# Kernel optimization log

Hardware: AMD Instinct MI355X
Metric: run time of the kernel (lower is better)

## Reference

```python
import jax, jax.numpy as jnp
import numpy as np

N_NODES = 100000
N_EDGES = 3200000
IN_FEATS = 128
OUT_FEATS = 16
NEG_SLOPE = 0.2


def setup_inputs() -> dict:
    key = jax.random.key(0)
    k1, k2, k3, k4, k5, k6 = jax.random.split(key, 6)
    h = jax.random.normal(k1, (N_NODES, IN_FEATS), dtype=jnp.float32)
    src = jax.random.randint(k2, (N_EDGES,), 0, N_NODES, dtype=jnp.int64)
    dst = jax.random.randint(k3, (N_EDGES,), 0, N_NODES, dtype=jnp.int64)
    W = jax.random.normal(k4, (OUT_FEATS, IN_FEATS), dtype=jnp.float32) * (1.0 / np.sqrt(IN_FEATS))
    a_l = jax.random.normal(k5, (1, OUT_FEATS), dtype=jnp.float32) * (1.0 / np.sqrt(OUT_FEATS))
    a_r = jax.random.normal(k6, (1, OUT_FEATS), dtype=jnp.float32) * (1.0 / np.sqrt(OUT_FEATS))
    return {"h": h, "src": src, "dst": dst, "W": W, "a_l": a_l, "a_r": a_r}


def reference(h, src, dst, W, a_l, a_r):
    N = h.shape[0]
    # node projection: h @ fc.weight.T  -> [N, out]
    hW = h @ W.T
    # per-node attention logits: [N, 1]
    el = hW @ a_l.T
    er = hW @ a_r.T
    # u_add_v: per-edge logit e = el[src] + er[dst], then leaky_relu(0.2)
    e = jax.nn.leaky_relu(el[src] + er[dst], negative_slope=NEG_SLOPE)  # [E, 1]
    # edge_softmax over edges grouped by destination node (numerically stable)
    emax = jax.ops.segment_max(e, dst, num_segments=N)  # [N, 1], -inf for empty
    emax = jnp.where(jnp.isfinite(emax), emax, 0.0)
    e_exp = jnp.exp(e - emax[dst])
    esum = jax.ops.segment_sum(e_exp, dst, num_segments=N)  # [N, 1]
    alpha = e_exp / jnp.maximum(esum[dst], 1e-16)  # [E, 1]
    # u_mul_e + sum: weighted aggregation of source features at destinations
    out = jax.ops.segment_sum(hW[src] * alpha, dst, num_segments=N)  # [N, out]
    return out
```

## Files before the change

kernel.cpp:

```cpp
#include <hip/hip_runtime.h>
#include <hip/hip_bf16.h>
#include <stdint.h>

#define IN_F 128
#define OUT_F 16
#define NEG_SLOPE 0.2f
#define SB_BITS 9
#define SB_NODES 512
#define NBS 196
#define CAP_SB 17408
#define TILE_NODES 128
#define LCAP 4608
#define SC_E 4096
#define W_LD (IN_F + 4)
#define SB_SPACING 200

#define SMEM_BYTES (3136 + 16384 + 4096)

__global__ __launch_bounds__(256) void proj_scatter_kernel(
    const float* __restrict__ h, const float* __restrict__ W,
    const float* __restrict__ a_l, const float* __restrict__ a_r,
    const int* __restrict__ src, const int* __restrict__ dst,
    float* __restrict__ hW, float* __restrict__ el, float* __restrict__ er,
    int* __restrict__ cursor, uint32_t* __restrict__ payload,
    int N, int E, int scatBlocks) {
  __shared__ __align__(16) uint8_t smem[SMEM_BYTES];
  int t = threadIdx.x;

  if ((int)blockIdx.x < scatBlocks) {
    int* hist = (int*)smem;
    int* pref = hist + NBS;
    int* gbase = pref + NBS;
    int* rank = gbase + NBS;
    uint32_t* sortedP = (uint32_t*)(smem + 3136);
    uint8_t* sortedB = smem + 3136 + 16384;

    int start = blockIdx.x * SC_E;
    int end = min(E, start + SC_E);
    int cnt = end - start;

    if (t < NBS) { hist[t] = 0; rank[t] = 0; }
    __syncthreads();

    for (int i = start + t; i < end; i += 256)
      atomicAdd(&hist[dst[i] >> SB_BITS], 1);
    __syncthreads();

    if (t == 0) {
      int run = 0;
      for (int b = 0; b < NBS; ++b) {
        pref[b] = run;
        run += hist[b];
      }
    }
    __syncthreads();
    if (t < NBS) {
      int c = hist[t];
      gbase[t] = c ? atomicAdd(&cursor[t * 16], c) : 0;
    }
    __syncthreads();

    for (int i = start + t; i < end; i += 256) {
      int d = dst[i];
      int s = src[i];
      int b = d >> SB_BITS;
      int r = atomicAdd(&rank[b], 1);
      int pos = pref[b] + r;
      sortedP[pos] = ((uint32_t)s << SB_BITS) | (uint32_t)(d & (SB_NODES - 1));
      sortedB[pos] = (uint8_t)b;
    }
    __syncthreads();

    for (int i = t; i < cnt; i += 256) {
      int b = sortedB[i];
      int ofs = gbase[b] + (i - pref[b]);
      if (ofs < CAP_SB) payload[(size_t)b * CAP_SB + ofs] = sortedP[i];
    }
  } else {
    float* Ws = (float*)smem;
    for (int i = t; i < OUT_F * IN_F; i += 256)
      Ws[(i >> 7) * W_LD + (i & (IN_F - 1))] = W[i];
    __syncthreads();

    int gid = ((int)blockIdx.x - scatBlocks) * 256 + t;
    int node = gid >> 4;
    int feat = gid & 15;
    if (node >= N) return;

    const float4* hrow = (const float4*)(h + (size_t)node * IN_F);
    const float4* wrow = (const float4*)(&Ws[feat * W_LD]);
    float acc = 0.f;
#pragma unroll
    for (int k = 0; k < IN_F / 4; ++k) {
      float4 hv = hrow[k];
      float4 wv = wrow[k];
      acc += hv.x * wv.x + hv.y * wv.y + hv.z * wv.z + hv.w * wv.w;
    }
    hW[node * OUT_F + feat] = acc;

    float vl = acc * a_l[feat];
    float vr = acc * a_r[feat];
#pragma unroll
    for (int off = 8; off; off >>= 1) {
      vl += __shfl_down(vl, off, 16);
      vr += __shfl_down(vr, off, 16);
    }
    if (feat == 0) {
      el[node] = vl;
      er[node] = vr;
    }
  }
}

__global__ __launch_bounds__(512) void agg_kernel(
    const uint32_t* __restrict__ payload, const int* __restrict__ cursor,
    const float* __restrict__ hW, const float* __restrict__ el,
    const float* __restrict__ er, float* __restrict__ out, int N) {
  __shared__ uint32_t sorted[LCAP];
  __shared__ float exS[LCAP];
  __shared__ int hist[TILE_NODES];
  __shared__ int pref[TILE_NODES];
  __shared__ int rank[TILE_NODES];

  int t = threadIdx.x;
  int sb = blockIdx.x % SB_SPACING;
  int quad = blockIdx.x / SB_SPACING;
  if (sb >= NBS) return;
  size_t base = (size_t)sb * CAP_SB;
  int cnt = min(cursor[sb * 16], CAP_SB);

  if (t < TILE_NODES) { hist[t] = 0; rank[t] = 0; }
  __syncthreads();

  const uint4* pay4 = (const uint4*)(payload + base);
  int n4 = (cnt + 3) >> 2;
  for (int i = t; i < n4; i += 512) {
    uint4 v = pay4[i];
    int i0 = i << 2;
    if (i0 + 0 < cnt && (int)((v.x >> 7) & 3) == quad) atomicAdd(&hist[v.x & (TILE_NODES - 1)], 1);
    if (i0 + 1 < cnt && (int)((v.y >> 7) & 3) == quad) atomicAdd(&hist[v.y & (TILE_NODES - 1)], 1);
    if (i0 + 2 < cnt && (int)((v.z >> 7) & 3) == quad) atomicAdd(&hist[v.z & (TILE_NODES - 1)], 1);
    if (i0 + 3 < cnt && (int)((v.w >> 7) & 3) == quad) atomicAdd(&hist[v.w & (TILE_NODES - 1)], 1);
  }
  __syncthreads();

  if (t < TILE_NODES) {
    int s = 0;
    for (int j = 0; j < t; ++j) s += hist[j];
    pref[t] = s;
  }
  __syncthreads();

  for (int i = t; i < n4; i += 512) {
    uint4 v = pay4[i];
    int i0 = i << 2;
#pragma unroll
    for (int j = 0; j < 4; ++j) {
      uint32_t p = j == 0 ? v.x : j == 1 ? v.y : j == 2 ? v.z : v.w;
      if (i0 + j < cnt && (int)((p >> 7) & 3) == quad) {
        int dl = (int)(p & (TILE_NODES - 1));
        int r = atomicAdd(&rank[dl], 1);
        int pos = pref[dl] + r;
        if (pos < LCAP) sorted[pos] = p;
      }
    }
  }
  __syncthreads();

  int node0 = sb * SB_NODES + quad * TILE_NODES;
  int kept = pref[TILE_NODES - 1] + hist[TILE_NODES - 1];
  for (int i = t; i < kept; i += 512) {
    uint32_t p = sorted[i];
    int s = (int)(p >> SB_BITS);
    float x = el[s] + er[node0 + (int)(p & (TILE_NODES - 1))];
    x = x > 0.f ? x : NEG_SLOPE * x;
    exS[i] = __expf(x);
  }
  __syncthreads();

  int g = t >> 4;
  int f = t & 15;
  for (int dl = g; dl < TILE_NODES; dl += 32) {
    int node = node0 + dl;
    if (node >= N) break;
    int k = pref[dl];
    int kend = k + hist[dl];
    float acc = 0.f;
    float es = 0.f;
#pragma unroll 4
    for (; k < kend; ++k) {
      float ex = exS[k];
      acc += ex * hW[(int)(sorted[k] >> SB_BITS) * OUT_F + f];
      es += ex;
    }
    out[(size_t)node * OUT_F + f] = acc / fmaxf(es, 1e-16f);
  }
}

extern "C" void kernel_launch(void* const* d_in, const int* in_sizes, int n_in,
                              void* d_out, int out_size, void* d_ws, size_t ws_size,
                              hipStream_t stream) {
  const float* h   = (const float*)d_in[0];
  const int*   src = (const int*)d_in[1];
  const int*   dst = (const int*)d_in[2];
  const float* W   = (const float*)d_in[3];
  const float* a_l = (const float*)d_in[4];
  const float* a_r = (const float*)d_in[5];
  float* out = (float*)d_out;

  const int N = in_sizes[0] / IN_F;
  const int E = in_sizes[1];
  const int scatBlocks = (E + SC_E - 1) / SC_E;
  const int projBlocks = (N * OUT_F + 255) / 256;

  float* ws = (float*)d_ws;
  float* hW = ws;
  float* el = hW + (size_t)N * OUT_F;
  float* er = el + N;
  int* cursor = (int*)(er + N);
  uint32_t* payload = (uint32_t*)(cursor + (size_t)NBS * 16);

  hipMemsetAsync(cursor, 0, (size_t)NBS * 16 * sizeof(int), stream);

  proj_scatter_kernel<<<scatBlocks + projBlocks, 256, 0, stream>>>(
      h, W, a_l, a_r, src, dst, hW, el, er, cursor, payload, N, E, scatBlocks);

  agg_kernel<<<SB_SPACING * 4, 512, 0, stream>>>(payload, cursor, hW, el, er,
                                                 out, N);
}
```

Before: 211.6 us.

## Replace per-tile counting sort with LDS atomic accumulation and vectorize scatter loads

The aggregation kernel no longer counting-sorts edges per destination within a tile. Kept edges are compacted with wavefront ballot and one atomic per wave, then each thread loads a full 16-float hW row and accumulates ex*hW and the exp sum into padded LDS rows with float atomics. This removes a histogram pass, a prefix scan and the serial per-node loop, at the cost of 17 LDS atomics per edge and possible contention on high-degree nodes. The scatter kernel also reads dst and src as int4 and computes the prefix in parallel per bucket instead of with a single thread.

New measurement: 531.6 us. 151% more time.

```diff
diff --git a/kernel.cpp b/kernel.cpp
--- a/kernel.cpp
+++ b/kernel.cpp
@@ -13,6 +13,7 @@
 #define LCAP 4608
 #define SC_E 4096
 #define W_LD (IN_F + 4)
+#define ACC_LD 17
 #define SB_SPACING 200
 
 #define SMEM_BYTES (3136 + 16384 + 4096)
@@ -42,31 +43,49 @@
     if (t < NBS) { hist[t] = 0; rank[t] = 0; }
     __syncthreads();
 
-    for (int i = start + t; i < end; i += 256)
+    const int4* dst4 = (const int4*)(dst + start);
+    int n4 = cnt >> 2;
+    for (int i = t; i < n4; i += 256) {
+      int4 d = dst4[i];
+      atomicAdd(&hist[d.x >> SB_BITS], 1);
+      atomicAdd(&hist[d.y >> SB_BITS], 1);
+      atomicAdd(&hist[d.z >> SB_BITS], 1);
+      atomicAdd(&hist[d.w >> SB_BITS], 1);
+    }
+    for (int i = start + (n4 << 2) + t; i < end; i += 256)
       atomicAdd(&hist[dst[i] >> SB_BITS], 1);
     __syncthreads();
 
-    if (t == 0) {
-      int run = 0;
-      for (int b = 0; b < NBS; ++b) {
-        pref[b] = run;
-        run += hist[b];
-      }
-    }
-    __syncthreads();
     if (t < NBS) {
+      int s = 0;
+      for (int j = 0; j < t; ++j) s += hist[j];
+      pref[t] = s;
       int c = hist[t];
       gbase[t] = c ? atomicAdd(&cursor[t * 16], c) : 0;
     }
     __syncthreads();
 
-    for (int i = start + t; i < end; i += 256) {
-      int d = dst[i];
-      int s = src[i];
-      int b = d >> SB_BITS;
+    const int4* src4 = (const int4*)(src + start);
+    for (int i = t; i < n4; i += 256) {
+      int4 d = dst4[i];
+      int4 s = src4[i];
+#pragma unroll
+      for (int j = 0; j < 4; ++j) {
+        int dd = j == 0 ? d.x : j == 1 ? d.y : j == 2 ? d.z : d.w;
+        int ss = j == 0 ? s.x : j == 1 ? s.y : j == 2 ? s.z : s.w;
+        int b = dd >> SB_BITS;
+        int r = atomicAdd(&rank[b], 1);
+        int pos = pref[b] + r;
+        sortedP[pos] = ((uint32_t)ss << SB_BITS) | (uint32_t)(dd & (SB_NODES - 1));
+        sortedB[pos] = (uint8_t)b;
+      }
+    }
+    for (int i = start + (n4 << 2) + t; i < end; i += 256) {
+      int dd = dst[i];
+      int b = dd >> SB_BITS;
       int r = atomicAdd(&rank[b], 1);
       int pos = pref[b] + r;
-      sortedP[pos] = ((uint32_t)s << SB_BITS) | (uint32_t)(d & (SB_NODES - 1));
+      sortedP[pos] = ((uint32_t)src[i] << SB_BITS) | (uint32_t)(dd & (SB_NODES - 1));
       sortedB[pos] = (uint8_t)b;
     }
     __syncthreads();
@@ -116,84 +135,85 @@
     const uint32_t* __restrict__ payload, const int* __restrict__ cursor,
     const float* __restrict__ hW, const float* __restrict__ el,
     const float* __restrict__ er, float* __restrict__ out, int N) {
-  __shared__ uint32_t sorted[LCAP];
-  __shared__ float exS[LCAP];
-  __shared__ int hist[TILE_NODES];
-  __shared__ int pref[TILE_NODES];
-  __shared__ int rank[TILE_NODES];
+  __shared__ uint32_t kept[LCAP];
+  __shared__ float accS[TILE_NODES * ACC_LD];
+  __shared__ float esumS[TILE_NODES];
+  __shared__ int kcnt;
 
   int t = threadIdx.x;
   int sb = blockIdx.x % SB_SPACING;
-  int quad = blockIdx.x / SB_SPACING;
+  uint32_t quad = blockIdx.x / SB_SPACING;
   if (sb >= NBS) return;
   size_t base = (size_t)sb * CAP_SB;
   int cnt = min(cursor[sb * 16], CAP_SB);
 
-  if (t < TILE_NODES) { hist[t] = 0; rank[t] = 0; }
+  for (int i = t; i < TILE_NODES * ACC_LD; i += 512) accS[i] = 0.f;
+  if (t < TILE_NODES) esumS[t] = 0.f;
+  if (t == 0) kcnt = 0;
   __syncthreads();
 
   const uint4* pay4 = (const uint4*)(payload + base);
   int n4 = (cnt + 3) >> 2;
+  int lane = t & 63;
   for (int i = t; i < n4; i += 512) {
     uint4 v = pay4[i];
     int i0 = i << 2;
-    if (i0 + 0 < cnt && (int)((v.x >> 7) & 3) == quad) atomicAdd(&hist[v.x & (TILE_NODES - 1)], 1);
-    if (i0 + 1 < cnt && (int)((v.y >> 7) & 3) == quad) atomicAdd(&hist[v.y & (TILE_NODES - 1)], 1);
-    if (i0 + 2 < cnt && (int)((v.z >> 7) & 3) == quad) atomicAdd(&hist[v.z & (TILE_NODES - 1)], 1);
-    if (i0 + 3 < cnt && (int)((v.w >> 7) & 3) == quad) atomicAdd(&hist[v.w & (TILE_NODES - 1)], 1);
-  }
-  __syncthreads();
-
-  if (t < TILE_NODES) {
-    int s = 0;
-    for (int j = 0; j < t; ++j) s += hist[j];
-    pref[t] = s;
-  }
-  __syncthreads();
-
-  for (int i = t; i < n4; i += 512) {
-    uint4 v = pay4[i];
-    int i0 = i << 2;
 #pragma unroll
     for (int j = 0; j < 4; ++j) {
       uint32_t p = j == 0 ? v.x : j == 1 ? v.y : j == 2 ? v.z : v.w;
-      if (i0 + j < cnt && (int)((p >> 7) & 3) == quad) {
-        int dl = (int)(p & (TILE_NODES - 1));
-        int r = atomicAdd(&rank[dl], 1);
-        int pos = pref[dl] + r;
-        if (pos < LCAP) sorted[pos] = p;
+      bool keep = (i0 + j < cnt) && (((p >> 7) & 3u) == quad);
+      unsigned long long m = __ballot(keep);
+      if (m) {
+        int leader = (int)(__ffsll((long long)m) - 1);
+        int bbase = 0;
+        if (lane == leader) bbase = atomicAdd(&kcnt, (int)__popcll(m));
+        bbase = __shfl(bbase, leader);
+        if (keep)
+          kept[bbase + (int)__popcll(m & ((1ull << lane) - 1))] = p;
       }
     }
   }
   __syncthreads();
-
-  int node0 = sb * SB_NODES + quad * TILE_NODES;
-  int kept = pref[TILE_NODES - 1] + hist[TILE_NODES - 1];
-  for (int i = t; i < kept; i += 512) {
-    uint32_t p = sorted[i];
+  int K = kcnt;
+
+  int node0 = sb * SB_NODES;
+  for (int i = t; i < K; i += 512) {
+    uint32_t p = kept[i];
     int s = (int)(p >> SB_BITS);
-    float x = el[s] + er[node0 + (int)(p & (TILE_NODES - 1))];
+    int dl = (int)(p & (SB_NODES - 1));
+    float x = el[s] + er[node0 + dl];
     x = x > 0.f ? x : NEG_SLOPE * x;
-    exS[i] = __expf(x);
+    float ex = __expf(x);
+    int tl = dl & (TILE_NODES - 1);
+    const float4* hw4 = (const float4*)(hW + (size_t)s * OUT_F);
+    float4 h0 = hw4[0], h1 = hw4[1], h2 = hw4[2], h3 = hw4[3];
+    float* arow = &accS[tl * ACC_LD];
+    atomicAdd(&arow[0],  ex * h0.x);
+    atomicAdd(&arow[1],  ex * h0.y);
+    atomicAdd(&arow[2],  ex * h0.z);
+    atomicAdd(&arow[3],  ex * h0.w);
+    atomicAdd(&arow[4],  ex * h1.x);
+    atomicAdd(&arow[5],  ex * h1.y);
+    atomicAdd(&arow[6],  ex * h1.z);
+    atomicAdd(&arow[7],  ex * h1.w);
+    atomicAdd(&arow[8],  ex * h2.x);
+    atomicAdd(&arow[9],  ex * h2.y);
+    atomicAdd(&arow[10], ex * h2.z);
+    atomicAdd(&arow[11], ex * h2.w);
+    atomicAdd(&arow[12], ex * h3.x);
+    atomicAdd(&arow[13], ex * h3.y);
+    atomicAdd(&arow[14], ex * h3.z);
+    atomicAdd(&arow[15], ex * h3.w);
+    atomicAdd(&esumS[tl], ex);
   }
   __syncthreads();
 
-  int g = t >> 4;
-  int f = t & 15;
-  for (int dl = g; dl < TILE_NODES; dl += 32) {
-    int node = node0 + dl;
-    if (node >= N) break;
-    int k = pref[dl];
-    int kend = k + hist[dl];
-    float acc = 0.f;
-    float es = 0.f;
-#pragma unroll 4
-    for (; k < kend; ++k) {
-      float ex = exS[k];
-      acc += ex * hW[(int)(sorted[k] >> SB_BITS) * OUT_F + f];
-      es += ex;
-    }
-    out[(size_t)node * OUT_F + f] = acc / fmaxf(es, 1e-16f);
+  int outBase = sb * SB_NODES + (int)quad * TILE_NODES;
+  int nlocal = min(TILE_NODES, N - outBase);
+  for (int i = t; i < nlocal * OUT_F; i += 512) {
+    int tl = i >> 4;
+    out[(size_t)outBase * OUT_F + i] =
+        accS[tl * ACC_LD + (i & 15)] / fmaxf(esumS[tl], 1e-16f);
   }
 }
 
```
